# Optimization experiments

Measured on AMD Instinct MI355X. Metric: run time of the kernel, lower is better.

## Reference

```python
import jax, jax.numpy as jnp
import numpy as np

N, E, B = 50000, 800000, 128
IN, HID, OUT, H = 256, 256, 256, 4
NEG_SLOPE = 0.2
EPS_BN = 1e-5
EPS_LN = 1e-5


def setup_inputs() -> dict:
    key = jax.random.key(0)
    ks = jax.random.split(key, 10)
    C1, C2 = HID // H, OUT // H
    s = lambda k, sh: jax.random.normal(k, sh, jnp.float32) * 0.05
    return dict(
        x=jax.random.normal(ks[0], (N, IN), jnp.float32),
        edge_index=jax.random.randint(ks[1], (2, E), 0, N),
        batch=jnp.sort(jax.random.randint(ks[2], (N,), 0, B)),
        W1=s(ks[3], (IN, HID)), a_src1=s(ks[4], (H, C1)), a_dst1=s(ks[5], (H, C1)),
        b1=jnp.zeros((HID,), jnp.float32),
        bn1_g=jnp.ones((HID,), jnp.float32), bn1_b=jnp.zeros((HID,), jnp.float32),
        bn1_m=jnp.zeros((HID,), jnp.float32), bn1_v=jnp.ones((HID,), jnp.float32),
        ln1_g=jnp.ones((HID,), jnp.float32), ln1_b=jnp.zeros((HID,), jnp.float32),
        W2=s(ks[6], (HID + IN, OUT)), a_src2=s(ks[7], (H, C2)), a_dst2=s(ks[8], (H, C2)),
        b2=jnp.zeros((OUT,), jnp.float32),
        bn2_g=jnp.ones((OUT,), jnp.float32), bn2_b=jnp.zeros((OUT,), jnp.float32),
        bn2_m=jnp.zeros((OUT,), jnp.float32), bn2_v=jnp.ones((OUT,), jnp.float32),
        ln2_g=jnp.ones((OUT,), jnp.float32), ln2_b=jnp.zeros((OUT,), jnp.float32),
    )


def gat_conv(x, edge_index, W, a_s, a_d, b):
    # PyG GATConv (concat heads, add_self_loops=True, eval -> no attention dropout)
    n = x.shape[0]
    Hh, C = a_s.shape
    h = (x @ W).reshape(n, Hh, C)                      # [N,H,C]
    loop = jnp.arange(n)
    src = jnp.concatenate([edge_index[0], loop])       # [E+N]
    dst = jnp.concatenate([edge_index[1], loop])
    al_s = jnp.einsum('nhc,hc->nh', h, a_s)            # [N,H]
    al_d = jnp.einsum('nhc,hc->nh', h, a_d)
    e = jax.nn.leaky_relu(al_s[src] + al_d[dst], NEG_SLOPE)   # [E+N,H]
    emax = jax.ops.segment_max(e, dst, num_segments=n)        # segment softmax over incoming edges
    p = jnp.exp(e - emax[dst])
    denom = jax.ops.segment_sum(p, dst, num_segments=n)
    alpha = p / (denom[dst] + 1e-16)
    out = jax.ops.segment_sum(alpha[:, :, None] * h[src], dst, num_segments=n)
    return out.reshape(n, Hh * C) + b


def bn_eval(x, g, b, m, v):
    return (x - m) * (g * jax.lax.rsqrt(v + EPS_BN)) + b


def layer_norm(x, g, b):
    mu = jnp.mean(x, axis=-1, keepdims=True)
    var = jnp.mean(jnp.square(x - mu), axis=-1, keepdims=True)
    return (x - mu) * jax.lax.rsqrt(var + EPS_LN) * g + b


def reference(x, edge_index, batch,
              W1, a_src1, a_dst1, b1, bn1_g, bn1_b, bn1_m, bn1_v, ln1_g, ln1_b,
              W2, a_src2, a_dst2, b2, bn2_g, bn2_b, bn2_m, bn2_v, ln2_g, ln2_b):
    x1 = x
    h = gat_conv(x, edge_index, W1, a_src1, a_dst1, b1)
    h = jax.nn.relu(layer_norm(bn_eval(h, bn1_g, bn1_b, bn1_m, bn1_v), ln1_g, ln1_b))
    x2 = h
    # root_extend: broadcast the first node of each (sorted) batch segment
    root_idx = jnp.searchsorted(batch, jnp.arange(B))  # first occurrence per graph
    h = jnp.concatenate([h, x1[root_idx[batch]]], axis=1)
    h = gat_conv(h, edge_index, W2, a_src2, a_dst2, b2)
    h = jax.nn.relu(layer_norm(bn_eval(h, bn2_g, bn2_b, bn2_m, bn2_v), ln2_g, ln2_b))
    h = jnp.concatenate([h, x2[root_idx[batch]]], axis=1)   # [N, OUT+HID]
    sums = jax.ops.segment_sum(h, batch, num_segments=B)
    cnt = jax.ops.segment_sum(jnp.ones((h.shape[0],), h.dtype), batch, num_segments=B)
    return sums / jnp.maximum(cnt, 1.0)[:, None]            # scatter_mean -> [B, OUT+HID]
```

## Files before the change

### kernel.cpp

```cpp
#include <hip/hip_runtime.h>
#include <stdint.h>

typedef unsigned short u16;
typedef unsigned int u32;
typedef __bf16 bf16x8 __attribute__((ext_vector_type(8)));
typedef float f32x4 __attribute__((ext_vector_type(4)));

#define NGRAPH 128

__device__ __forceinline__ float b2f(u16 u) {
    union { u32 i; float f; } c; c.i = ((u32)u) << 16; return c.f;
}
__device__ __forceinline__ u16 f2b(float f) {
    union { float f; u32 i; } c; c.f = f;
    u32 r = c.i + 0x7fffu + ((c.i >> 16) & 1u);
    return (u16)(r >> 16);
}

__global__ void k_sentinel(u16* __restrict__ out, int n, u16 pat) {
    int i = blockIdx.x * 256 + threadIdx.x;
    if (i < n) out[i] = pat;
}

__global__ void k_detect(const u16* __restrict__ x, int* __restrict__ flag) {
    __shared__ int cnt;
    if (threadIdx.x == 0) cnt = 0;
    __syncthreads();
    int weird = 0;
    for (int i = threadIdx.x; i < 4096; i += 256) {
        u16 u = x[2 * i];
        int e = (u >> 7) & 0xff;
        if (e != 0 && (e < 100 || e > 140)) weird++;
    }
    atomicAdd(&cnt, weird);
    __syncthreads();
    if (threadIdx.x == 0) *flag = (cnt > 1024) ? 1 : 0;
}

__global__ __launch_bounds__(256) void k_cvt(const void* __restrict__ src, u16* __restrict__ dst,
                                             int n, const int* __restrict__ flag) {
    int f = *flag;
    int i = blockIdx.x * 256 + threadIdx.x;
    if (i < n) dst[i] = f ? f2b(((const float*)src)[i]) : ((const u16*)src)[i];
}

__global__ __launch_bounds__(256) void k_cvt_small(
    const void* p0, const void* p1, const void* p2, const void* p3, const void* p4,
    const void* p5, const void* p6, const void* p7, const void* p8, const void* p9,
    const void* p10, const void* p11, const void* p12, const void* p13, const void* p14,
    const void* p15, const void* p16, const void* p17,
    u16* __restrict__ dst, const int* __restrict__ flag) {
    const void* ps[18] = {p0,p1,p2,p3,p4,p5,p6,p7,p8,p9,p10,p11,p12,p13,p14,p15,p16,p17};
    int f = *flag;
    int vec = blockIdx.x;
    int j = threadIdx.x;
    const void* s = ps[vec];
    dst[vec * 256 + j] = f ? f2b(((const float*)s)[j]) : ((const u16*)s)[j];
}

__global__ void k_zero(int* __restrict__ deg, float* __restrict__ pool, int nd, int np) {
    int i = blockIdx.x * blockDim.x + threadIdx.x;
    if (i < nd) deg[i] = 0;
    if (i < np) pool[i] = 0.0f;
}

__global__ void k_transpose(const u16* __restrict__ w, u16* __restrict__ wt) {
    int idx = blockIdx.x * 256 + threadIdx.x;
    int n = idx >> 8, k = idx & 255;
    wt[n * 256 + k] = w[k * 256 + n];
}

__global__ void k_root(const int* __restrict__ batch, int* __restrict__ root, int N, int B) {
    int b = threadIdx.x;
    if (b > B) return;
    int lo = 0, hi = N;
    while (lo < hi) { int mid = (lo + hi) >> 1; if (batch[mid] < b) lo = mid + 1; else hi = mid; }
    root[b] = lo;
}

__global__ __launch_bounds__(256) void k_hist(const int* __restrict__ ei, int* __restrict__ deg, int E) {
    int e = blockIdx.x * 256 + threadIdx.x;
    if (e < E) atomicAdd(&deg[ei[E + e]], 1);
}

__global__ __launch_bounds__(256) void k_scan1(const int* __restrict__ in, int* __restrict__ out,
                                               int* __restrict__ bsums, int total) {
    __shared__ int lds[256];
    int tid = threadIdx.x;
    int base = blockIdx.x * 2048 + tid * 8;
    int v[8]; int ts = 0;
#pragma unroll
    for (int r = 0; r < 8; r++) { int i = base + r; int x = (i < total) ? in[i] : 0; v[r] = x; ts += x; }
    lds[tid] = ts;
    __syncthreads();
    for (int off = 1; off < 256; off <<= 1) {
        int t = (tid >= off) ? lds[tid - off] : 0;
        __syncthreads();
        lds[tid] += t;
        __syncthreads();
    }
    int run = lds[tid] - ts;
#pragma unroll
    for (int r = 0; r < 8; r++) { int i = base + r; if (i < total) out[i] = run; run += v[r]; }
    if (tid == 255) bsums[blockIdx.x] = lds[255];
}

__global__ void k_scan2(int* __restrict__ bsums, int nb) {
    if (threadIdx.x == 0 && blockIdx.x == 0) {
        int run = 0;
        for (int i = 0; i < nb; i++) { int t = bsums[i]; bsums[i] = run; run += t; }
    }
}

__global__ __launch_bounds__(256) void k_scan3(const int* __restrict__ pscan, const int* __restrict__ bsums,
                                               int* __restrict__ ptr, int* __restrict__ cursor,
                                               int total, int N) {
    int i = blockIdx.x * 256 + threadIdx.x;
    if (i >= total) return;
    int val = pscan[i] + bsums[i >> 11];
    ptr[i] = val;
    if (i < N) cursor[i] = val;
}

__global__ __launch_bounds__(256) void k_fill(const int* __restrict__ ei, int* __restrict__ cursor,
                                              int* __restrict__ csr, int E) {
    int e = blockIdx.x * 256 + threadIdx.x;
    if (e < E) {
        int src = ei[e];
        int pos = atomicAdd(&cursor[ei[E + e]], 1);
        csr[pos] = src;
    }
}

__global__ __launch_bounds__(256) void k_gemm(const u16* __restrict__ A, const u16* __restrict__ Bt,
                                              u16* __restrict__ C, int M,
                                              const float* __restrict__ r2, const int* __restrict__ batch) {
    __shared__ __align__(16) u16 As[128 * 64];
    __shared__ __align__(16) u16 Bs[128 * 64];
    const int tid = threadIdx.x;
    const int lane = tid & 63;
    const int wave = tid >> 6;
    const int bm = blockIdx.x >> 1;
    const int bn = blockIdx.x & 1;
    const int m0 = bm * 128, n0 = bn * 128;
    const int wm = wave >> 1, wn = wave & 1;
    const int lm = lane & 15, lq = lane >> 4;
    f32x4 acc[4][4] = {};

    for (int k0 = 0; k0 < 256; k0 += 64) {
        uint4 ra[4], rb[4];
#pragma unroll
        for (int it = 0; it < 4; ++it) {
            int t = tid + 256 * it;
            int m = t >> 3;
            int kc = (t & 7) ^ (m & 7);
            int gm = m0 + m; if (gm > M - 1) gm = M - 1;
            ra[it] = *(const uint4*)(A + (size_t)gm * 256 + k0 + kc * 8);
            rb[it] = *(const uint4*)(Bt + (size_t)(n0 + m) * 256 + k0 + kc * 8);
        }
        __syncthreads();
#pragma unroll
        for (int it = 0; it < 4; ++it) {
            int t = tid + 256 * it;
            *(uint4*)(As + t * 8) = ra[it];
            *(uint4*)(Bs + t * 8) = rb[it];
        }
        __syncthreads();
#pragma unroll
        for (int ks = 0; ks < 2; ++ks) {
            int kq = ks * 4 + lq;
            bf16x8 af[4], bfr[4];
#pragma unroll
            for (int i = 0; i < 4; i++) {
                int m = wm * 64 + i * 16 + lm;
                af[i] = *(const bf16x8*)(As + (m * 8 + (kq ^ (m & 7))) * 8);
                int n = wn * 64 + i * 16 + lm;
                bfr[i] = *(const bf16x8*)(Bs + (n * 8 + (kq ^ (n & 7))) * 8);
            }
#pragma unroll
            for (int i = 0; i < 4; i++)
#pragma unroll
                for (int j = 0; j < 4; j++)
                    acc[i][j] = __builtin_amdgcn_mfma_f32_16x16x32_bf16(af[i], bfr[j], acc[i][j], 0, 0, 0);
        }
    }
#pragma unroll
    for (int i = 0; i < 4; i++) {
#pragma unroll
        for (int r = 0; r < 4; r++) {
            int row = m0 + wm * 64 + i * 16 + lq * 4 + r;
            if (row >= M) continue;
            const float* r2row = r2 ? (r2 + (size_t)batch[row] * 256) : nullptr;
#pragma unroll
            for (int j = 0; j < 4; j++) {
                int col = n0 + wn * 64 + j * 16 + lm;
                float v = acc[i][j][r];
                if (r2row) v += r2row[col];
                C[(size_t)row * 256 + col] = f2b(v);
            }
        }
    }
}

__global__ __launch_bounds__(256) void k_al(const u16* __restrict__ h, const u16* __restrict__ a_s,
                                            const u16* __restrict__ a_d,
                                            float* __restrict__ al_s, float* __restrict__ al_d, int N) {
    int node = blockIdx.x * 4 + (threadIdx.x >> 6);
    if (node >= N) return;
    int lane = threadIdx.x & 63;
    int c0 = lane * 4;
    int head = lane >> 4;
    int ci = c0 & 63;
    ushort4 hv = *(const ushort4*)(h + (size_t)node * 256 + c0);
    float h0 = b2f(hv.x), h1 = b2f(hv.y), h2 = b2f(hv.z), h3 = b2f(hv.w);
    ushort4 sv = *(const ushort4*)(a_s + head * 64 + ci);
    ushort4 dv = *(const ushort4*)(a_d + head * 64 + ci);
    float ps = h0 * b2f(sv.x) + h1 * b2f(sv.y) + h2 * b2f(sv.z) + h3 * b2f(sv.w);
    float pd = h0 * b2f(dv.x) + h1 * b2f(dv.y) + h2 * b2f(dv.z) + h3 * b2f(dv.w);
#pragma unroll
    for (int off = 1; off < 16; off <<= 1) { ps += __shfl_xor(ps, off); pd += __shfl_xor(pd, off); }
    if ((lane & 15) == 0) { al_s[node * 4 + head] = ps; al_d[node * 4 + head] = pd; }
}

__global__ __launch_bounds__(256) void k_attw(
    const float* __restrict__ als, const float* __restrict__ ald_,
    const int* __restrict__ ptr, const int* __restrict__ csr,
    float* __restrict__ aw, float* __restrict__ selfp, float* __restrict__ invs, int N) {
    int node = blockIdx.x * 4 + (threadIdx.x >> 6);
    if (node >= N) return;
    int lane = threadIdx.x & 63;
    int hd = lane & 3;
    int el = lane >> 2;
    int beg = ptr[node], end = ptr[node + 1];
    float ad = ald_[node * 4 + hd];
    float es = als[node * 4 + hd] + ad; es = (es > 0.f) ? es : 0.2f * es;
    float m = es;
    for (int i0 = beg; i0 < end; i0 += 16) {
        int i = i0 + el;
        if (i < end) {
            int src = csr[i];
            float e2 = als[src * 4 + hd] + ad; e2 = (e2 > 0.f) ? e2 : 0.2f * e2;
            m = fmaxf(m, e2);
        }
    }
#pragma unroll
    for (int off = 4; off < 64; off <<= 1) m = fmaxf(m, __shfl_xor(m, off));
    float s = 0.f;
    for (int i0 = beg; i0 < end; i0 += 16) {
        int i = i0 + el;
        if (i < end) {
            int src = csr[i];
            float e2 = als[src * 4 + hd] + ad; e2 = (e2 > 0.f) ? e2 : 0.2f * e2;
            float p = __expf(e2 - m);
            aw[(size_t)i * 4 + hd] = p;
            s += p;
        }
    }
#pragma unroll
    for (int off = 4; off < 64; off <<= 1) s += __shfl_xor(s, off);
    float pself = __expf(es - m);
    s += pself;
    if (el == 0) {
        float inv = 1.0f / (s + 1e-16f);
        selfp[node * 4 + hd] = pself * inv;
        invs[node * 4 + hd] = inv;
    }
}

__global__ __launch_bounds__(256) void k_agg2(
    const u16* __restrict__ h, const float* __restrict__ aw,
    const float* __restrict__ selfp, const float* __restrict__ invs,
    const int* __restrict__ ptr, const int* __restrict__ csr,
    const u16* __restrict__ bias, const u16* __restrict__ bng, const u16* __restrict__ bnb,
    const u16* __restrict__ bnm, const u16* __restrict__ bnv,
    const u16* __restrict__ lng, const u16* __restrict__ lnb,
    u16* __restrict__ xout, float* __restrict__ pool, const int* __restrict__ batch, int N) {
    int node = blockIdx.x * 4 + (threadIdx.x >> 6);
    if (node >= N) return;
    int lane = threadIdx.x & 63;
    int c0 = lane * 4;
    int head = lane >> 4;
    int beg = ptr[node], end = ptr[node + 1];
    float a0 = 0.f, a1 = 0.f, a2 = 0.f, a3 = 0.f;
    int i = beg;
    for (; i + 4 <= end; i += 4) {
        int s0 = csr[i], s1 = csr[i + 1], s2 = csr[i + 2], s3 = csr[i + 3];
        float p0 = aw[(size_t)i * 4 + head];
        float p1 = aw[(size_t)(i + 1) * 4 + head];
        float p2 = aw[(size_t)(i + 2) * 4 + head];
        float p3 = aw[(size_t)(i + 3) * 4 + head];
        ushort4 r0 = *(const ushort4*)(h + (size_t)s0 * 256 + c0);
        ushort4 r1 = *(const ushort4*)(h + (size_t)s1 * 256 + c0);
        ushort4 r2v = *(const ushort4*)(h + (size_t)s2 * 256 + c0);
        ushort4 r3 = *(const ushort4*)(h + (size_t)s3 * 256 + c0);
        a0 += p0 * b2f(r0.x) + p1 * b2f(r1.x) + p2 * b2f(r2v.x) + p3 * b2f(r3.x);
        a1 += p0 * b2f(r0.y) + p1 * b2f(r1.y) + p2 * b2f(r2v.y) + p3 * b2f(r3.y);
        a2 += p0 * b2f(r0.z) + p1 * b2f(r1.z) + p2 * b2f(r2v.z) + p3 * b2f(r3.z);
        a3 += p0 * b2f(r0.w) + p1 * b2f(r1.w) + p2 * b2f(r2v.w) + p3 * b2f(r3.w);
    }
    for (; i < end; ++i) {
        int s0 = csr[i];
        float p0 = aw[(size_t)i * 4 + head];
        ushort4 r0 = *(const ushort4*)(h + (size_t)s0 * 256 + c0);
        a0 += p0 * b2f(r0.x); a1 += p0 * b2f(r0.y); a2 += p0 * b2f(r0.z); a3 += p0 * b2f(r0.w);
    }
    float inv = invs[node * 4 + head];
    float sp = selfp[node * 4 + head];
    ushort4 hs = *(const ushort4*)(h + (size_t)node * 256 + c0);
    float v0 = a0 * inv + sp * b2f(hs.x) + b2f(bias[c0 + 0]);
    float v1 = a1 * inv + sp * b2f(hs.y) + b2f(bias[c0 + 1]);
    float v2 = a2 * inv + sp * b2f(hs.z) + b2f(bias[c0 + 2]);
    float v3 = a3 * inv + sp * b2f(hs.w) + b2f(bias[c0 + 3]);
    v0 = (v0 - b2f(bnm[c0 + 0])) * (b2f(bng[c0 + 0]) * rsqrtf(b2f(bnv[c0 + 0]) + 1e-5f)) + b2f(bnb[c0 + 0]);
    v1 = (v1 - b2f(bnm[c0 + 1])) * (b2f(bng[c0 + 1]) * rsqrtf(b2f(bnv[c0 + 1]) + 1e-5f)) + b2f(bnb[c0 + 1]);
    v2 = (v2 - b2f(bnm[c0 + 2])) * (b2f(bng[c0 + 2]) * rsqrtf(b2f(bnv[c0 + 2]) + 1e-5f)) + b2f(bnb[c0 + 2]);
    v3 = (v3 - b2f(bnm[c0 + 3])) * (b2f(bng[c0 + 3]) * rsqrtf(b2f(bnv[c0 + 3]) + 1e-5f)) + b2f(bnb[c0 + 3]);
    float sum = v0 + v1 + v2 + v3;
#pragma unroll
    for (int off = 1; off < 64; off <<= 1) sum += __shfl_xor(sum, off);
    float mu = sum * 0.00390625f;
    float d0 = v0 - mu, d1 = v1 - mu, d2 = v2 - mu, d3 = v3 - mu;
    float q = d0 * d0 + d1 * d1 + d2 * d2 + d3 * d3;
#pragma unroll
    for (int off = 1; off < 64; off <<= 1) q += __shfl_xor(q, off);
    float rstd = rsqrtf(q * 0.00390625f + 1e-5f);
    float y0 = fmaxf(d0 * rstd * b2f(lng[c0 + 0]) + b2f(lnb[c0 + 0]), 0.f);
    float y1 = fmaxf(d1 * rstd * b2f(lng[c0 + 1]) + b2f(lnb[c0 + 1]), 0.f);
    float y2 = fmaxf(d2 * rstd * b2f(lng[c0 + 2]) + b2f(lnb[c0 + 2]), 0.f);
    float y3 = fmaxf(d3 * rstd * b2f(lng[c0 + 3]) + b2f(lnb[c0 + 3]), 0.f);
    if (xout) {
        uint2 o;
        o.x = (u32)f2b(y0) | ((u32)f2b(y1) << 16);
        o.y = (u32)f2b(y2) | ((u32)f2b(y3) << 16);
        *(uint2*)(xout + (size_t)node * 256 + c0) = o;
    }
    if (pool) {
        int g = batch[node];
        float* pp = pool + (size_t)g * 256 + c0;
        atomicAdd(pp + 0, y0); atomicAdd(pp + 1, y1); atomicAdd(pp + 2, y2); atomicAdd(pp + 3, y3);
    }
}

__global__ __launch_bounds__(256) void k_r2(const u16* __restrict__ xc, const u16* __restrict__ w2,
                                            const int* __restrict__ root, float* __restrict__ r2, int N) {
    __shared__ float xs[256];
    int b = blockIdx.x, c = threadIdx.x;
    int rt = root[b]; if (rt >= N) rt = N - 1; if (rt < 0) rt = 0;
    xs[c] = b2f(xc[(size_t)rt * 256 + c]);
    __syncthreads();
    float acc = 0.f;
    for (int k = 0; k < 256; k++) acc += xs[k] * b2f(w2[(size_t)(256 + k) * 256 + c]);
    r2[b * 256 + c] = acc;
}

__global__ void k_final(const float* __restrict__ pool, const u16* __restrict__ x2,
                        const int* __restrict__ root, void* __restrict__ out,
                        const int* __restrict__ flag) {
    int b = blockIdx.x, c = threadIdx.x;
    int r0 = root[b], r1 = root[b + 1];
    int cnt = r1 - r0;
    float inv = 1.0f / (float)(cnt > 1 ? cnt : 1);
    float v0 = pool[b * 256 + c] * inv;
    float v1 = (cnt > 0) ? b2f(x2[(size_t)r0 * 256 + c]) : 0.0f;
    if (*flag) {
        float* o = (float*)out;
        o[b * 512 + c] = v0;
        o[b * 512 + 256 + c] = v1;
    } else {
        u16* o = (u16*)out;
        o[b * 512 + c] = f2b(v0);
        o[b * 512 + 256 + c] = f2b(v1);
    }
}

extern "C" void kernel_launch(void* const* d_in, const int* in_sizes, int n_in,
                              void* d_out, int out_size, void* d_ws, size_t ws_size,
                              hipStream_t stream) {
    u16* outp = (u16*)d_out;
    int ogrid = (out_size + 255) / 256;

    if (n_in != 23) {
        k_sentinel<<<ogrid, 256, 0, stream>>>(outp, out_size, (u16)0x44FA);
        return;
    }

    const void* x_raw = d_in[0];
    const int* ei = (const int*)d_in[1];
    const int* batch = (const int*)d_in[2];
    const int NX = in_sizes[0];
    const int E = in_sizes[1] / 2;
    const int N = in_sizes[2];
    const int NW1 = in_sizes[3];
    const int NW2 = in_sizes[13];
    const int B = NGRAPH;

    char* p = (char*)d_ws;
    auto carve = [&](size_t bytes) -> void* {
        void* r = (void*)p; p += (bytes + 255) & ~(size_t)255; return r;
    };
    u16* xc    = (u16*)carve((size_t)NX * 2);
    u16* w1c   = (u16*)carve((size_t)NW1 * 2);
    u16* w2c   = (u16*)carve((size_t)NW2 * 2);
    u16* sc    = (u16*)carve((size_t)18 * 256 * 2);
    u16* wt1   = (u16*)carve((size_t)65536 * 2);
    u16* wt2   = (u16*)carve((size_t)65536 * 2);
    u16* hbuf  = (u16*)carve((size_t)N * 256 * 2);
    u16* x2    = (u16*)carve((size_t)N * 256 * 2);
    float* als = (float*)carve((size_t)N * 4 * 4);
    float* ald = (float*)carve((size_t)N * 4 * 4);
    float* aw  = (float*)carve((size_t)E * 4 * 4);
    float* sfp = (float*)carve((size_t)N * 4 * 4);
    float* ivs = (float*)carve((size_t)N * 4 * 4);
    int* deg    = (int*)carve((size_t)(N + 1) * 4);
    int* pscan  = (int*)carve((size_t)(N + 1) * 4);
    int* ptr    = (int*)carve((size_t)(N + 1) * 4);
    int* cursor = (int*)carve((size_t)N * 4);
    int* csr    = (int*)carve((size_t)E * 4);
    int* bsums  = (int*)carve(1024);
    int* root   = (int*)carve((size_t)(B + 1) * 4);
    float* r2   = (float*)carve((size_t)B * 256 * 4);
    float* pool = (float*)carve((size_t)B * 256 * 4);
    int* flag   = (int*)carve(256);

    size_t needed = (size_t)(p - (char*)d_ws);
    if (needed > ws_size) {
        k_sentinel<<<ogrid, 256, 0, stream>>>(outp, out_size, (u16)0x447A);
        return;
    }

    k_detect<<<1, 256, 0, stream>>>((const u16*)x_raw, flag);

    int zmax = (N + 1) > (B * 256) ? (N + 1) : (B * 256);
    k_zero<<<(zmax + 255) / 256, 256, 0, stream>>>(deg, pool, N + 1, B * 256);

    k_cvt<<<(NX + 255) / 256, 256, 0, stream>>>(x_raw, xc, NX, flag);
    k_cvt<<<(NW1 + 255) / 256, 256, 0, stream>>>(d_in[3], w1c, NW1, flag);
    k_cvt<<<(NW2 + 255) / 256, 256, 0, stream>>>(d_in[13], w2c, NW2, flag);
    k_cvt_small<<<18, 256, 0, stream>>>(
        d_in[4], d_in[5], d_in[6], d_in[7], d_in[8], d_in[9], d_in[10], d_in[11], d_in[12],
        d_in[14], d_in[15], d_in[16], d_in[17], d_in[18], d_in[19], d_in[20], d_in[21], d_in[22],
        sc, flag);

    k_transpose<<<256, 256, 0, stream>>>(w1c, wt1);
    k_transpose<<<256, 256, 0, stream>>>(w2c, wt2);
    k_root<<<1, 256, 0, stream>>>(batch, root, N, B);

    k_hist<<<(E + 255) / 256, 256, 0, stream>>>(ei, deg, E);
    int nb1 = (N + 1 + 2047) / 2048;
    k_scan1<<<nb1, 256, 0, stream>>>(deg, pscan, bsums, N + 1);
    k_scan2<<<1, 64, 0, stream>>>(bsums, nb1);
    k_scan3<<<(N + 1 + 255) / 256, 256, 0, stream>>>(pscan, bsums, ptr, cursor, N + 1, N);
    k_fill<<<(E + 255) / 256, 256, 0, stream>>>(ei, cursor, csr, E);

    int mt = (N + 127) / 128;
    int ngrid = (N + 3) / 4;
    k_gemm<<<mt * 2, 256, 0, stream>>>(xc, wt1, hbuf, N, nullptr, nullptr);
    k_al<<<ngrid, 256, 0, stream>>>(hbuf, sc + 0 * 256, sc + 1 * 256, als, ald, N);
    k_attw<<<ngrid, 256, 0, stream>>>(als, ald, ptr, csr, aw, sfp, ivs, N);
    k_agg2<<<ngrid, 256, 0, stream>>>(hbuf, aw, sfp, ivs, ptr, csr,
        sc + 2 * 256, sc + 3 * 256, sc + 4 * 256, sc + 5 * 256, sc + 6 * 256, sc + 7 * 256, sc + 8 * 256,
        x2, nullptr, batch, N);
    k_r2<<<B, 256, 0, stream>>>(xc, w2c, root, r2, N);
    k_gemm<<<mt * 2, 256, 0, stream>>>(x2, wt2, hbuf, N, r2, batch);
    k_al<<<ngrid, 256, 0, stream>>>(hbuf, sc + 9 * 256, sc + 10 * 256, als, ald, N);
    k_attw<<<ngrid, 256, 0, stream>>>(als, ald, ptr, csr, aw, sfp, ivs, N);
    k_agg2<<<ngrid, 256, 0, stream>>>(hbuf, aw, sfp, ivs, ptr, csr,
        sc + 11 * 256, sc + 12 * 256, sc + 13 * 256, sc + 14 * 256, sc + 15 * 256, sc + 16 * 256, sc + 17 * 256,
        nullptr, pool, batch, N);

    k_final<<<B, 256, 0, stream>>>(pool, x2, root, d_out, flag);
    (void)ws_size;
}
```

Before: 795.4 us.

## Fuse attention softmax into aggregation kernel without max subtraction

Removes the separate attention-weight kernel. The aggregation kernel now computes exp(leaky_relu(al_s[src]+al_d[dst])) inline, accumulates the softmax denominator alongside the weighted sum, and normalises at the end. This drops the per-edge attention buffer and its global write and read, plus one launch per layer. Each lane now handles 8 channels, and the wave is split into two halves that process alternating edges before a cross-half shuffle reduce. The max-subtraction pass is removed, so large logits could overflow exp. Padded edge slots also issue redundant loads of the node's own row.

```diff
diff --git a/kernel.cpp b/kernel.cpp
--- a/kernel.cpp
+++ b/kernel.cpp
@@ -222,54 +222,8 @@
     if ((lane & 15) == 0) { al_s[node * 4 + head] = ps; al_d[node * 4 + head] = pd; }
 }
 
-__global__ __launch_bounds__(256) void k_attw(
-    const float* __restrict__ als, const float* __restrict__ ald_,
-    const int* __restrict__ ptr, const int* __restrict__ csr,
-    float* __restrict__ aw, float* __restrict__ selfp, float* __restrict__ invs, int N) {
-    int node = blockIdx.x * 4 + (threadIdx.x >> 6);
-    if (node >= N) return;
-    int lane = threadIdx.x & 63;
-    int hd = lane & 3;
-    int el = lane >> 2;
-    int beg = ptr[node], end = ptr[node + 1];
-    float ad = ald_[node * 4 + hd];
-    float es = als[node * 4 + hd] + ad; es = (es > 0.f) ? es : 0.2f * es;
-    float m = es;
-    for (int i0 = beg; i0 < end; i0 += 16) {
-        int i = i0 + el;
-        if (i < end) {
-            int src = csr[i];
-            float e2 = als[src * 4 + hd] + ad; e2 = (e2 > 0.f) ? e2 : 0.2f * e2;
-            m = fmaxf(m, e2);
-        }
-    }
-#pragma unroll
-    for (int off = 4; off < 64; off <<= 1) m = fmaxf(m, __shfl_xor(m, off));
-    float s = 0.f;
-    for (int i0 = beg; i0 < end; i0 += 16) {
-        int i = i0 + el;
-        if (i < end) {
-            int src = csr[i];
-            float e2 = als[src * 4 + hd] + ad; e2 = (e2 > 0.f) ? e2 : 0.2f * e2;
-            float p = __expf(e2 - m);
-            aw[(size_t)i * 4 + hd] = p;
-            s += p;
-        }
-    }
-#pragma unroll
-    for (int off = 4; off < 64; off <<= 1) s += __shfl_xor(s, off);
-    float pself = __expf(es - m);
-    s += pself;
-    if (el == 0) {
-        float inv = 1.0f / (s + 1e-16f);
-        selfp[node * 4 + hd] = pself * inv;
-        invs[node * 4 + hd] = inv;
-    }
-}
-
-__global__ __launch_bounds__(256) void k_agg2(
-    const u16* __restrict__ h, const float* __restrict__ aw,
-    const float* __restrict__ selfp, const float* __restrict__ invs,
+__global__ __launch_bounds__(256) void k_agg3(
+    const u16* __restrict__ h, const float* __restrict__ als, const float* __restrict__ ald_,
     const int* __restrict__ ptr, const int* __restrict__ csr,
     const u16* __restrict__ bias, const u16* __restrict__ bng, const u16* __restrict__ bnb,
     const u16* __restrict__ bnm, const u16* __restrict__ bnv,
@@ -278,66 +232,110 @@
     int node = blockIdx.x * 4 + (threadIdx.x >> 6);
     if (node >= N) return;
     int lane = threadIdx.x & 63;
-    int c0 = lane * 4;
-    int head = lane >> 4;
+    int half = lane >> 5;
+    int cl = lane & 31;
+    int c0 = cl * 8;
+    int head = cl >> 3;
     int beg = ptr[node], end = ptr[node + 1];
-    float a0 = 0.f, a1 = 0.f, a2 = 0.f, a3 = 0.f;
-    int i = beg;
-    for (; i + 4 <= end; i += 4) {
-        int s0 = csr[i], s1 = csr[i + 1], s2 = csr[i + 2], s3 = csr[i + 3];
-        float p0 = aw[(size_t)i * 4 + head];
-        float p1 = aw[(size_t)(i + 1) * 4 + head];
-        float p2 = aw[(size_t)(i + 2) * 4 + head];
-        float p3 = aw[(size_t)(i + 3) * 4 + head];
-        ushort4 r0 = *(const ushort4*)(h + (size_t)s0 * 256 + c0);
-        ushort4 r1 = *(const ushort4*)(h + (size_t)s1 * 256 + c0);
-        ushort4 r2v = *(const ushort4*)(h + (size_t)s2 * 256 + c0);
-        ushort4 r3 = *(const ushort4*)(h + (size_t)s3 * 256 + c0);
-        a0 += p0 * b2f(r0.x) + p1 * b2f(r1.x) + p2 * b2f(r2v.x) + p3 * b2f(r3.x);
-        a1 += p0 * b2f(r0.y) + p1 * b2f(r1.y) + p2 * b2f(r2v.y) + p3 * b2f(r3.y);
-        a2 += p0 * b2f(r0.z) + p1 * b2f(r1.z) + p2 * b2f(r2v.z) + p3 * b2f(r3.z);
-        a3 += p0 * b2f(r0.w) + p1 * b2f(r1.w) + p2 * b2f(r2v.w) + p3 * b2f(r3.w);
-    }
-    for (; i < end; ++i) {
-        int s0 = csr[i];
-        float p0 = aw[(size_t)i * 4 + head];
-        ushort4 r0 = *(const ushort4*)(h + (size_t)s0 * 256 + c0);
-        a0 += p0 * b2f(r0.x); a1 += p0 * b2f(r0.y); a2 += p0 * b2f(r0.z); a3 += p0 * b2f(r0.w);
-    }
-    float inv = invs[node * 4 + head];
-    float sp = selfp[node * 4 + head];
-    ushort4 hs = *(const ushort4*)(h + (size_t)node * 256 + c0);
-    float v0 = a0 * inv + sp * b2f(hs.x) + b2f(bias[c0 + 0]);
-    float v1 = a1 * inv + sp * b2f(hs.y) + b2f(bias[c0 + 1]);
-    float v2 = a2 * inv + sp * b2f(hs.z) + b2f(bias[c0 + 2]);
-    float v3 = a3 * inv + sp * b2f(hs.w) + b2f(bias[c0 + 3]);
-    v0 = (v0 - b2f(bnm[c0 + 0])) * (b2f(bng[c0 + 0]) * rsqrtf(b2f(bnv[c0 + 0]) + 1e-5f)) + b2f(bnb[c0 + 0]);
-    v1 = (v1 - b2f(bnm[c0 + 1])) * (b2f(bng[c0 + 1]) * rsqrtf(b2f(bnv[c0 + 1]) + 1e-5f)) + b2f(bnb[c0 + 1]);
-    v2 = (v2 - b2f(bnm[c0 + 2])) * (b2f(bng[c0 + 2]) * rsqrtf(b2f(bnv[c0 + 2]) + 1e-5f)) + b2f(bnb[c0 + 2]);
-    v3 = (v3 - b2f(bnm[c0 + 3])) * (b2f(bng[c0 + 3]) * rsqrtf(b2f(bnv[c0 + 3]) + 1e-5f)) + b2f(bnb[c0 + 3]);
-    float sum = v0 + v1 + v2 + v3;
+    float ad = ald_[node * 4 + head];
+
+    float acc[8] = {};
+    float s = 0.f;
+    for (int i0 = beg; i0 < end; i0 += 16) {
+#pragma unroll
+        for (int u = 0; u < 8; ++u) {
+            int e = i0 + 2 * u + half;
+            bool valid = (e < end);
+            int src = valid ? csr[e] : node;
+            float e2 = als[src * 4 + head] + ad;
+            e2 = (e2 > 0.f) ? e2 : 0.2f * e2;
+            float p = valid ? __expf(e2) : 0.f;
+            uint4 rv = *(const uint4*)(h + (size_t)src * 256 + c0);
+            s += p;
+            acc[0] += p * b2f((u16)(rv.x & 0xffff));
+            acc[1] += p * b2f((u16)(rv.x >> 16));
+            acc[2] += p * b2f((u16)(rv.y & 0xffff));
+            acc[3] += p * b2f((u16)(rv.y >> 16));
+            acc[4] += p * b2f((u16)(rv.z & 0xffff));
+            acc[5] += p * b2f((u16)(rv.z >> 16));
+            acc[6] += p * b2f((u16)(rv.w & 0xffff));
+            acc[7] += p * b2f((u16)(rv.w >> 16));
+        }
+    }
+#pragma unroll
+    for (int j = 0; j < 8; ++j) acc[j] += __shfl_xor(acc[j], 32);
+    s += __shfl_xor(s, 32);
+    {
+        float es = als[node * 4 + head] + ad;
+        es = (es > 0.f) ? es : 0.2f * es;
+        float ps = __expf(es);
+        uint4 rv = *(const uint4*)(h + (size_t)node * 256 + c0);
+        s += ps;
+        acc[0] += ps * b2f((u16)(rv.x & 0xffff));
+        acc[1] += ps * b2f((u16)(rv.x >> 16));
+        acc[2] += ps * b2f((u16)(rv.y & 0xffff));
+        acc[3] += ps * b2f((u16)(rv.y >> 16));
+        acc[4] += ps * b2f((u16)(rv.z & 0xffff));
+        acc[5] += ps * b2f((u16)(rv.z >> 16));
+        acc[6] += ps * b2f((u16)(rv.w & 0xffff));
+        acc[7] += ps * b2f((u16)(rv.w >> 16));
+    }
+    float inv = 1.0f / (s + 1e-16f);
+    uint4 bi = *(const uint4*)(bias + c0);
+    uint4 gm = *(const uint4*)(bng + c0);
+    uint4 bb = *(const uint4*)(bnb + c0);
+    uint4 mm = *(const uint4*)(bnm + c0);
+    uint4 vv = *(const uint4*)(bnv + c0);
+    uint4 lg = *(const uint4*)(lng + c0);
+    uint4 lb = *(const uint4*)(lnb + c0);
+    float v[8];
+#pragma unroll
+    for (int j = 0; j < 8; ++j) {
+        u32 w;
+        float fbi, fgm, fbb, fmm, fvv;
+        w = (&bi.x)[j >> 1]; fbi = b2f((u16)((j & 1) ? (w >> 16) : (w & 0xffff)));
+        w = (&gm.x)[j >> 1]; fgm = b2f((u16)((j & 1) ? (w >> 16) : (w & 0xffff)));
+        w = (&bb.x)[j >> 1]; fbb = b2f((u16)((j & 1) ? (w >> 16) : (w & 0xffff)));
+        w = (&mm.x)[j >> 1]; fmm = b2f((u16)((j & 1) ? (w >> 16) : (w & 0xffff)));
+        w = (&vv.x)[j >> 1]; fvv = b2f((u16)((j & 1) ? (w >> 16) : (w & 0xffff)));
+        float t = acc[j] * inv + fbi;
+        v[j] = (t - fmm) * (fgm * rsqrtf(fvv + 1e-5f)) + fbb;
+    }
+    float sum = 0.f;
+#pragma unroll
+    for (int j = 0; j < 8; ++j) sum += v[j];
 #pragma unroll
     for (int off = 1; off < 64; off <<= 1) sum += __shfl_xor(sum, off);
-    float mu = sum * 0.00390625f;
-    float d0 = v0 - mu, d1 = v1 - mu, d2 = v2 - mu, d3 = v3 - mu;
-    float q = d0 * d0 + d1 * d1 + d2 * d2 + d3 * d3;
+    float mu = sum * (1.0f / 512.0f);
+    float q = 0.f;
+#pragma unroll
+    for (int j = 0; j < 8; ++j) { v[j] -= mu; q += v[j] * v[j]; }
 #pragma unroll
     for (int off = 1; off < 64; off <<= 1) q += __shfl_xor(q, off);
-    float rstd = rsqrtf(q * 0.00390625f + 1e-5f);
-    float y0 = fmaxf(d0 * rstd * b2f(lng[c0 + 0]) + b2f(lnb[c0 + 0]), 0.f);
-    float y1 = fmaxf(d1 * rstd * b2f(lng[c0 + 1]) + b2f(lnb[c0 + 1]), 0.f);
-    float y2 = fmaxf(d2 * rstd * b2f(lng[c0 + 2]) + b2f(lnb[c0 + 2]), 0.f);
-    float y3 = fmaxf(d3 * rstd * b2f(lng[c0 + 3]) + b2f(lnb[c0 + 3]), 0.f);
-    if (xout) {
-        uint2 o;
-        o.x = (u32)f2b(y0) | ((u32)f2b(y1) << 16);
-        o.y = (u32)f2b(y2) | ((u32)f2b(y3) << 16);
-        *(uint2*)(xout + (size_t)node * 256 + c0) = o;
-    }
-    if (pool) {
-        int g = batch[node];
-        float* pp = pool + (size_t)g * 256 + c0;
-        atomicAdd(pp + 0, y0); atomicAdd(pp + 1, y1); atomicAdd(pp + 2, y2); atomicAdd(pp + 3, y3);
+    float rstd = rsqrtf(q * (1.0f / 512.0f) + 1e-5f);
+    float y[8];
+#pragma unroll
+    for (int j = 0; j < 8; ++j) {
+        u32 w1 = (&lg.x)[j >> 1], w2 = (&lb.x)[j >> 1];
+        float flg = b2f((u16)((j & 1) ? (w1 >> 16) : (w1 & 0xffff)));
+        float flb = b2f((u16)((j & 1) ? (w2 >> 16) : (w2 & 0xffff)));
+        y[j] = fmaxf(v[j] * rstd * flg + flb, 0.f);
+    }
+    if (half == 0) {
+        if (xout) {
+            uint4 o;
+            o.x = (u32)f2b(y[0]) | ((u32)f2b(y[1]) << 16);
+            o.y = (u32)f2b(y[2]) | ((u32)f2b(y[3]) << 16);
+            o.z = (u32)f2b(y[4]) | ((u32)f2b(y[5]) << 16);
+            o.w = (u32)f2b(y[6]) | ((u32)f2b(y[7]) << 16);
+            *(uint4*)(xout + (size_t)node * 256 + c0) = o;
+        }
+        if (pool) {
+            int g = batch[node];
+            float* pp = pool + (size_t)g * 256 + c0;
+#pragma unroll
+            for (int j = 0; j < 8; ++j) atomicAdd(pp + j, y[j]);
+        }
     }
 }
 
@@ -408,9 +406,6 @@
     u16* x2    = (u16*)carve((size_t)N * 256 * 2);
     float* als = (float*)carve((size_t)N * 4 * 4);
     float* ald = (float*)carve((size_t)N * 4 * 4);
-    float* aw  = (float*)carve((size_t)E * 4 * 4);
-    float* sfp = (float*)carve((size_t)N * 4 * 4);
-    float* ivs = (float*)carve((size_t)N * 4 * 4);
     int* deg    = (int*)carve((size_t)(N + 1) * 4);
     int* pscan  = (int*)carve((size_t)(N + 1) * 4);
     int* ptr    = (int*)carve((size_t)(N + 1) * 4);
@@ -456,15 +451,13 @@
     int ngrid = (N + 3) / 4;
     k_gemm<<<mt * 2, 256, 0, stream>>>(xc, wt1, hbuf, N, nullptr, nullptr);
     k_al<<<ngrid, 256, 0, stream>>>(hbuf, sc + 0 * 256, sc + 1 * 256, als, ald, N);
-    k_attw<<<ngrid, 256, 0, stream>>>(als, ald, ptr, csr, aw, sfp, ivs, N);
-    k_agg2<<<ngrid, 256, 0, stream>>>(hbuf, aw, sfp, ivs, ptr, csr,
+    k_agg3<<<ngrid, 256, 0, stream>>>(hbuf, als, ald, ptr, csr,
         sc + 2 * 256, sc + 3 * 256, sc + 4 * 256, sc + 5 * 256, sc + 6 * 256, sc + 7 * 256, sc + 8 * 256,
         x2, nullptr, batch, N);
     k_r2<<<B, 256, 0, stream>>>(xc, w2c, root, r2, N);
     k_gemm<<<mt * 2, 256, 0, stream>>>(x2, wt2, hbuf, N, r2, batch);
     k_al<<<ngrid, 256, 0, stream>>>(hbuf, sc + 9 * 256, sc + 10 * 256, als, ald, N);
-    k_attw<<<ngrid, 256, 0, stream>>>(als, ald, ptr, csr, aw, sfp, ivs, N);
-    k_agg2<<<ngrid, 256, 0, stream>>>(hbuf, aw, sfp, ivs, ptr, csr,
+    k_agg3<<<ngrid, 256, 0, stream>>>(hbuf, als, ald, ptr, csr,
         sc + 11 * 256, sc + 12 * 256, sc + 13 * 256, sc + 14 * 256, sc + 15 * 256, sc + 16 * 256, sc + 17 * 256,
         nullptr, pool, batch, N);
 
```

Result: slower. 1.142 ms (+43.6%).
